# Kernel optimization log

Measured on AMD Instinct MI355X. Metric: run time of the kernel, lower is better.

The kernel has to match this reference:

```python
import jax, jax.numpy as jnp
import numpy as np

N_NODES = 50000
N_EDGES = 600000
N_GRAPHS = 512
IN_C, HID_C, OUT_C = 128, 128, 64


def setup_inputs() -> dict:
    key = jax.random.key(0)
    ks = jax.random.split(key, 16)
    inp = {
        "x": jax.random.normal(ks[0], (N_NODES, IN_C), dtype=jnp.float32),
        "edge_index": jax.random.randint(ks[1], (2, N_EDGES), 0, N_NODES, dtype=jnp.int64),
        "batch": jnp.sort(jax.random.randint(ks[2], (N_NODES,), 0, N_GRAPHS, dtype=jnp.int64)),
    }
    # GINConv MLPs: Linear(din,dout) -> ReLU -> Linear(dout,dout)
    dims = [(IN_C, HID_C), (HID_C, HID_C), (HID_C, OUT_C)]
    ki = 3
    for l, (din, dout) in enumerate(dims):
        inp[f"w1_{l}"] = jax.random.normal(ks[ki], (din, dout), jnp.float32) / np.sqrt(din).astype(np.float32)
        inp[f"b1_{l}"] = jnp.zeros((dout,), jnp.float32)
        inp[f"w2_{l}"] = jax.random.normal(ks[ki + 1], (dout, dout), jnp.float32) / np.sqrt(dout).astype(np.float32)
        inp[f"b2_{l}"] = jnp.zeros((dout,), jnp.float32)
        ki += 2
    return inp


def _gin_conv(x, src, dst, w1, b1, w2, b2):
    # sum-aggregate neighbor features: agg[i] = sum_{(j->i) in E} x[j]
    agg = jax.ops.segment_sum(x[src], dst, num_segments=N_NODES)
    h = x + agg  # eps = 0 -> (1+eps)*x + agg
    h = jnp.maximum(h @ w1 + b1, 0.0)
    return h @ w2 + b2


def reference(x, edge_index, batch,
              w1_0, b1_0, w2_0, b2_0,
              w1_1, b1_1, w2_1, b2_1,
              w1_2, b1_2, w2_2, b2_2):
    src, dst = edge_index[0], edge_index[1]
    params = [(w1_0, b1_0, w2_0, b2_0),
              (w1_1, b1_1, w2_1, b2_1),
              (w1_2, b1_2, w2_2, b2_2)]
    # first num_layers-1 convs with outer ReLU
    for l in range(2):
        x = jnp.maximum(_gin_conv(x, src, dst, *params[l]), 0.0)
    x = _gin_conv(x, src, dst, *params[2])
    # global_add_pool over graph ids -> [G, out_channels]
    return jax.ops.segment_sum(x, batch, num_segments=N_GRAPHS)
```

## Files before the change

kernel.cpp:

```cpp
#include <hip/hip_runtime.h>

#define N_NODES 50000
#define N_EDGES 600000
#define N_GRAPHS 512
#define CAP 48
#define NRT 3125

typedef unsigned int u32;
typedef unsigned short u16;
typedef __attribute__((ext_vector_type(8))) short bf16x8;
typedef __attribute__((ext_vector_type(4))) float f32x4;

__device__ __forceinline__ float bflo(u32 v) { return __uint_as_float(v << 16); }
__device__ __forceinline__ float bfhi(u32 v) { return __uint_as_float(v & 0xffff0000u); }
__device__ __forceinline__ u16 f2bf(float f) {
    u32 x = __float_as_uint(f);
    return (u16)((x + 0x7fffu + ((x >> 16) & 1u)) >> 16);
}
__device__ __forceinline__ void addrow(float* a, uint4 v) {
    a[0] += bflo(v.x); a[1] += bfhi(v.x);
    a[2] += bflo(v.y); a[3] += bfhi(v.y);
    a[4] += bflo(v.z); a[5] += bfhi(v.z);
    a[6] += bflo(v.w); a[7] += bfhi(v.w);
}
__device__ __forceinline__ void addrow2(float* a, uint2 v) {
    a[0] += bflo(v.x); a[1] += bfhi(v.x);
    a[2] += bflo(v.y); a[3] += bfhi(v.y);
}

__device__ __forceinline__ int idx_at(const int* __restrict__ a, int i, int wide) {
    return wide ? a[2 * i] : a[i];
}

__global__ void init_kernel(const int* __restrict__ ei, int* __restrict__ cnt,
                            int* __restrict__ flag, float* __restrict__ out,
                            int out_n) {
    int i = blockIdx.x * 256 + threadIdx.x;
    if (i < N_NODES) cnt[i] = 0;
    if (i < out_n) out[i] = 0.f;
    if (blockIdx.x == 0 && threadIdx.x < 64) {
        int v = ei[2 * threadIdx.x + 1];
        unsigned long long nz = __ballot(v != 0);
        if (threadIdx.x == 0) *flag = (nz == 0ull) ? 1 : 0;
    }
}

struct CvtDesc { const float* w; u16* wt; int K, N, bx, bstart; };
struct CvtAll { CvtDesc d[6]; };
struct PrepArgs {
    const int* ei; const int* flag;
    int* cnt; int* slots;
    const float* x; u16* xb;
    CvtAll ca;
};
#define SCAT_B 2344
#define CVTX_B 6250
#define PREP_B (SCAT_B + CVTX_B + 76)

__global__ void prep_kernel(PrepArgs p) {
    int b = blockIdx.x;
    if (b < SCAT_B) {
        int e = b * 256 + threadIdx.x;
        if (e >= N_EDGES) return;
        int w = *p.flag;
        const int* src = p.ei;
        const int* dst = p.ei + (w ? 2 * N_EDGES : N_EDGES);
        int d = idx_at(dst, e, w);
        int pos = atomicAdd(&p.cnt[d], 1);
        if (pos < CAP) p.slots[(size_t)d * CAP + pos] = idx_at(src, e, w);
        return;
    }
    if (b < SCAT_B + CVTX_B) {
        size_t i = (size_t)(b - SCAT_B) * 256 + threadIdx.x;
        float4 v = *(const float4*)&p.x[i * 4];
        u32 o0 = (u32)f2bf(v.x) | ((u32)f2bf(v.y) << 16);
        u32 o1 = (u32)f2bf(v.z) | ((u32)f2bf(v.w) << 16);
        uint2 o; o.x = o0; o.y = o1;
        *(uint2*)&p.xb[i * 4] = o;
        return;
    }
    __shared__ float tile[32][33];
    int rel0 = b - (SCAT_B + CVTX_B);
    int di = 0;
#pragma unroll
    for (int i = 1; i < 6; ++i) if (rel0 >= p.ca.d[i].bstart) di = i;
    CvtDesc d = p.ca.d[di];
    int rel = rel0 - d.bstart;
    int bk = (rel % d.bx) * 32, bn = (rel / d.bx) * 32;
    int tx = threadIdx.x & 31, ty = threadIdx.x >> 5;
#pragma unroll
    for (int yy = 0; yy < 32; yy += 8)
        tile[ty + yy][tx] = d.w[(size_t)(bk + ty + yy) * d.N + bn + tx];
    __syncthreads();
#pragma unroll
    for (int yy = 0; yy < 32; yy += 8)
        d.wt[(size_t)(bn + ty + yy) * d.K + bk + tx] = f2bf(tile[tx][ty + yy]);
}

__global__ void agg128_kernel(const u16* __restrict__ xb, const int* __restrict__ cnt,
                              const int* __restrict__ slots, u16* __restrict__ h2) {
    int node = blockIdx.x * 16 + (threadIdx.x >> 4);
    int l = threadIdx.x & 15;
    if (node >= N_NODES) return;
    uint4 sv = *(const uint4*)(xb + ((size_t)node << 7) + l * 8);
    float acc[8] = { bflo(sv.x), bfhi(sv.x), bflo(sv.y), bfhi(sv.y),
                     bflo(sv.z), bfhi(sv.z), bflo(sv.w), bfhi(sv.w) };
    int deg = cnt[node]; if (deg > CAP) deg = CAP;
    const int* sp = slots + (size_t)node * CAP;
    int j = 0;
    for (; j + 4 <= deg; j += 4) {
        int s0 = sp[j], s1 = sp[j + 1], s2 = sp[j + 2], s3 = sp[j + 3];
        uint4 v0 = *(const uint4*)(xb + ((size_t)s0 << 7) + l * 8);
        uint4 v1 = *(const uint4*)(xb + ((size_t)s1 << 7) + l * 8);
        uint4 v2 = *(const uint4*)(xb + ((size_t)s2 << 7) + l * 8);
        uint4 v3 = *(const uint4*)(xb + ((size_t)s3 << 7) + l * 8);
        addrow(acc, v0); addrow(acc, v1);
        addrow(acc, v2); addrow(acc, v3);
    }
    for (; j < deg; ++j) {
        int s0 = sp[j];
        uint4 v0 = *(const uint4*)(xb + ((size_t)s0 << 7) + l * 8);
        addrow(acc, v0);
    }
    uint4 o;
    o.x = (u32)f2bf(acc[0]) | ((u32)f2bf(acc[1]) << 16);
    o.y = (u32)f2bf(acc[2]) | ((u32)f2bf(acc[3]) << 16);
    o.z = (u32)f2bf(acc[4]) | ((u32)f2bf(acc[5]) << 16);
    o.w = (u32)f2bf(acc[6]) | ((u32)f2bf(acc[7]) << 16);
    *(uint4*)(h2 + (size_t)(node >> 4) * 2048 + l * 128 + (node & 15) * 8) = o;
}

__global__ void agg64_kernel(const u16* __restrict__ z, const int* __restrict__ cnt,
                             const int* __restrict__ slots,
                             const float* __restrict__ b1, u16* __restrict__ tout) {
    int node = blockIdx.x * 16 + (threadIdx.x >> 4);
    int l = threadIdx.x & 15;
    if (node >= N_NODES) return;
    uint2 sv = *(const uint2*)(z + ((size_t)node << 6) + l * 4);
    float acc[4] = { bflo(sv.x), bfhi(sv.x), bflo(sv.y), bfhi(sv.y) };
    int deg = cnt[node]; if (deg > CAP) deg = CAP;
    const int* sp = slots + (size_t)node * CAP;
    int j = 0;
    for (; j + 4 <= deg; j += 4) {
        int s0 = sp[j], s1 = sp[j + 1], s2 = sp[j + 2], s3 = sp[j + 3];
        uint2 v0 = *(const uint2*)(z + ((size_t)s0 << 6) + l * 4);
        uint2 v1 = *(const uint2*)(z + ((size_t)s1 << 6) + l * 4);
        uint2 v2 = *(const uint2*)(z + ((size_t)s2 << 6) + l * 4);
        uint2 v3 = *(const uint2*)(z + ((size_t)s3 << 6) + l * 4);
        addrow2(acc, v0); addrow2(acc, v1);
        addrow2(acc, v2); addrow2(acc, v3);
    }
    for (; j < deg; ++j) {
        int s0 = sp[j];
        uint2 v0 = *(const uint2*)(z + ((size_t)s0 << 6) + l * 4);
        addrow2(acc, v0);
    }
    float t0 = fmaxf(acc[0] + b1[l * 4 + 0], 0.f);
    float t1 = fmaxf(acc[1] + b1[l * 4 + 1], 0.f);
    float t2 = fmaxf(acc[2] + b1[l * 4 + 2], 0.f);
    float t3 = fmaxf(acc[3] + b1[l * 4 + 3], 0.f);
    uint2 o;
    o.x = (u32)f2bf(t0) | ((u32)f2bf(t1) << 16);
    o.y = (u32)f2bf(t2) | ((u32)f2bf(t3) << 16);
    *(uint2*)(tout + ((size_t)node << 6) + l * 4) = o;
}

template <int CHAIN>
__global__ __launch_bounds__(256) void mlp_kernel(
    const u16* __restrict__ h2,
    const u16* __restrict__ w1t, const float* __restrict__ b1,
    const u16* __restrict__ w2t, const float* __restrict__ b2,
    const u16* __restrict__ w3t, u16* __restrict__ zout,
    u16* __restrict__ yout)
{
    __shared__ __attribute__((aligned(16))) u16 ts[4 * 2048];
    __shared__ __attribute__((aligned(16))) u16 ys[4 * 2048];
    const int wave = threadIdx.x >> 6, lane = threadIdx.x & 63;
    const int rtile = blockIdx.x * 4 + wave;
    if (rtile >= NRT) return;
    const int m = lane & 15, q = lane >> 4, ko = q * 8;
    u16* tsw = ts + wave * 2048;
    u16* ysw = ys + wave * 2048;
    const u16* hp = h2 + (size_t)rtile * 2048;

    bf16x8 a1[4];
#pragma unroll
    for (int s = 0; s < 4; ++s)
        a1[s] = *(const bf16x8*)&hp[s * 512 + q * 128 + m * 8];

    {
        f32x4 acc[8];
#pragma unroll
        for (int nt = 0; nt < 8; ++nt) acc[nt] = (f32x4){0.f, 0.f, 0.f, 0.f};
#pragma unroll
        for (int nt = 0; nt < 8; ++nt) {
            int n = nt * 16 + m;
#pragma unroll
            for (int s = 0; s < 4; ++s) {
                bf16x8 bf = *(const bf16x8*)&w1t[(size_t)n * 128 + s * 32 + ko];
                acc[nt] = __builtin_amdgcn_mfma_f32_16x16x32_bf16(a1[s], bf, acc[nt], 0, 0, 0);
            }
        }
#pragma unroll
        for (int nt = 0; nt < 8; ++nt) {
            int n = nt * 16 + m;
            float bias = b1[n];
#pragma unroll
            for (int j2 = 0; j2 < 4; ++j2) {
                int dr = q * 4 + j2;
                float v = fmaxf(acc[nt][j2] + bias, 0.f);
                tsw[dr * 128 + (n ^ ((dr & 7) << 3))] = f2bf(v);
            }
        }
    }

    {
        const int sw = (m & 7) << 3;
        bf16x8 a2[4];
#pragma unroll
        for (int s = 0; s < 4; ++s)
            a2[s] = *(const bf16x8*)&tsw[m * 128 + ((s * 32 + ko) ^ sw)];
        f32x4 acc[8];
#pragma unroll
        for (int nt = 0; nt < 8; ++nt) acc[nt] = (f32x4){0.f, 0.f, 0.f, 0.f};
#pragma unroll
        for (int nt = 0; nt < 8; ++nt) {
            int n = nt * 16 + m;
#pragma unroll
            for (int s = 0; s < 4; ++s) {
                bf16x8 bf = *(const bf16x8*)&w2t[(size_t)n * 128 + s * 32 + ko];
                acc[nt] = __builtin_amdgcn_mfma_f32_16x16x32_bf16(a2[s], bf, acc[nt], 0, 0, 0);
            }
        }
#pragma unroll
        for (int nt = 0; nt < 8; ++nt) {
            int n = nt * 16 + m;
            float bias = b2[n];
#pragma unroll
            for (int j2 = 0; j2 < 4; ++j2) {
                int dr = q * 4 + j2;
                float v = fmaxf(acc[nt][j2] + bias, 0.f);
                ysw[dr * 128 + (n ^ ((dr & 7) << 3))] = f2bf(v);
            }
        }
    }

    if (CHAIN) {
        const int sw = (m & 7) << 3;
        bf16x8 a3[4];
#pragma unroll
        for (int s = 0; s < 4; ++s)
            a3[s] = *(const bf16x8*)&ysw[m * 128 + ((s * 32 + ko) ^ sw)];
        f32x4 acc3[4];
#pragma unroll
        for (int nt = 0; nt < 4; ++nt) acc3[nt] = (f32x4){0.f, 0.f, 0.f, 0.f};
#pragma unroll
        for (int nt = 0; nt < 4; ++nt) {
            int n3 = nt * 16 + m;
#pragma unroll
            for (int s = 0; s < 4; ++s) {
                bf16x8 bf = *(const bf16x8*)&w3t[(size_t)n3 * 128 + s * 32 + ko];
                acc3[nt] = __builtin_amdgcn_mfma_f32_16x16x32_bf16(a3[s], bf, acc3[nt], 0, 0, 0);
            }
        }
#pragma unroll
        for (int nt = 0; nt < 4; ++nt) {
            int n3 = nt * 16 + m;
#pragma unroll
            for (int j2 = 0; j2 < 4; ++j2) {
                int row = q * 4 + j2;
                zout[(size_t)(rtile * 16 + row) * 64 + n3] = f2bf(acc3[nt][j2]);
            }
        }
    } else {
        int r = lane >> 2;
        int c0 = (lane & 3) * 32;
        const int sw = (r & 7) << 3;
#pragma unroll
        for (int j = 0; j < 4; ++j) {
            int ce = c0 + j * 8;
            uint4 v = *(const uint4*)&ysw[r * 128 + (ce ^ sw)];
            *(uint4*)&yout[(size_t)(rtile * 16 + r) * 128 + ce] = v;
        }
    }
}

__global__ __launch_bounds__(1024) void pool_kernel(
    const u16* __restrict__ t, const u16* __restrict__ w2t,
    const float* __restrict__ b2,
    const int* __restrict__ batch, const int* __restrict__ flagp,
    float* __restrict__ out)
{
    constexpr int YB_ST = 66;
    __shared__ __attribute__((aligned(16))) char smemA[64 * YB_ST * 4];
    __shared__ int gids[64];
    u16* hs = (u16*)smemA;
    float* yb = (float*)smemA;

    const int tid = threadIdx.x;
    const int wave = tid >> 6, lane = tid & 63;
    const int base = blockIdx.x * 64;
    const int wflag = *flagp;

    if (tid < 64) {
        int node = base + tid;
        gids[tid] = (node < N_NODES) ? idx_at(batch, node, wflag) : -1;
    }
    {
        int row = tid >> 4, c0 = (tid & 15) * 4;
        uint2 v = *(const uint2*)&t[((size_t)(base + row)) * 64 + c0];
        *(uint2*)&hs[row * 64 + (c0 ^ ((row & 7) << 3))] = v;
    }
    __syncthreads();

    const int m = lane & 15;
    const int ko = (lane >> 4) * 8;
    const int rb = (wave & 3) * 16;
    const int cb = (wave >> 2) * 16;

    {
        const int rr = rb + m;
        const int sw = (rr & 7) << 3;
        bf16x8 a2[2];
#pragma unroll
        for (int s = 0; s < 2; ++s)
            a2[s] = *(const bf16x8*)&hs[rr * 64 + ((s * 32 + ko) ^ sw)];
        f32x4 acc = (f32x4){0.f, 0.f, 0.f, 0.f};
        int n = cb + m;
#pragma unroll
        for (int s = 0; s < 2; ++s) {
            bf16x8 bf = *(const bf16x8*)&w2t[(size_t)n * 64 + s * 32 + ko];
            acc = __builtin_amdgcn_mfma_f32_16x16x32_bf16(a2[s], bf, acc, 0, 0, 0);
        }
        float bias = b2[n];
        __syncthreads();
#pragma unroll
        for (int j2 = 0; j2 < 4; ++j2) {
            int dr = rb + (lane >> 4) * 4 + j2;
            yb[dr * YB_ST + n] = acc[j2] + bias;
        }
    }
    __syncthreads();

    {
        int gl = gids[lane];
        int gp = (lane > 0) ? gids[lane - 1] : gl;
        unsigned long long mask = __ballot(lane > 0 && gl != gp) | 1ull;
        int nruns = (int)__popcll(mask);
        int c = tid >> 4, s = tid & 15;
        unsigned long long mm = mask;
        for (int r = 0; r < nruns; ++r) {
            int start = (int)__builtin_ctzll(mm);
            mm &= mm - 1;
            int end = mm ? (int)__builtin_ctzll(mm) : 64;
            int gid = gids[start];
            if (gid >= 0) {
                float sum = 0.f;
                for (int n2 = start + s; n2 < end; n2 += 16)
                    sum += yb[n2 * YB_ST + c];
                sum += __shfl_xor(sum, 1);
                sum += __shfl_xor(sum, 2);
                sum += __shfl_xor(sum, 4);
                sum += __shfl_xor(sum, 8);
                if (s == 0)
                    atomicAdd(&out[(size_t)gid * 64 + c], sum);
            }
        }
    }
}

extern "C" void kernel_launch(void* const* d_in, const int* in_sizes, int n_in,
                              void* d_out, int out_size, void* d_ws, size_t ws_size,
                              hipStream_t stream) {
    const float* x     = (const float*)d_in[0];
    const int*   ei    = (const int*)d_in[1];
    const int*   batch = (const int*)d_in[2];
    const float* w1[3] = {(const float*)d_in[3], (const float*)d_in[7],  (const float*)d_in[11]};
    const float* b1[3] = {(const float*)d_in[4], (const float*)d_in[8],  (const float*)d_in[12]};
    const float* w2[3] = {(const float*)d_in[5], (const float*)d_in[9],  (const float*)d_in[13]};
    const float* b2[3] = {(const float*)d_in[6], (const float*)d_in[10], (const float*)d_in[14]};
    float* out = (float*)d_out;

    char* ws = (char*)d_ws;
    int*   cnt     = (int*)(ws + 0);
    int*   flag    = (int*)(ws + 200704);
    int*   slots   = (int*)(ws + 201728);
    u16*   xb      = (u16*)(ws + 9801728);
    u16*   hbuf    = (u16*)(ws + 22601728);
    u16*   yA      = (u16*)(ws + 35401728);
    u16*   wts     = (u16*)(ws + 48201728);
    u16*   zbuf    = xb;
    u16*   tbuf    = yA;
    u16* w1t0 = wts +      0;
    u16* w2t0 = wts +  16384;
    u16* w1t1 = wts +  32768;
    u16* w2t1 = wts +  49152;
    u16* w1t2 = wts +  65536;
    u16* w2t2 = wts +  73728;

    init_kernel<<<196, 256, 0, stream>>>(ei, cnt, flag, out, out_size);

    PrepArgs pa;
    pa.ei = ei; pa.flag = flag; pa.cnt = cnt; pa.slots = slots;
    pa.x = x; pa.xb = xb;
    pa.ca.d[0] = {w1[0], w1t0, 128, 128, 4,  0};
    pa.ca.d[1] = {w2[0], w2t0, 128, 128, 4, 16};
    pa.ca.d[2] = {w1[1], w1t1, 128, 128, 4, 32};
    pa.ca.d[3] = {w2[1], w2t1, 128, 128, 4, 48};
    pa.ca.d[4] = {w1[2], w1t2, 128,  64, 4, 64};
    pa.ca.d[5] = {w2[2], w2t2,  64,  64, 2, 72};
    prep_kernel<<<PREP_B, 256, 0, stream>>>(pa);

    const int NAGG = (N_NODES + 15) / 16;
    const int NTIL = (N_NODES + 63) / 64;

    agg128_kernel<<<NAGG, 256, 0, stream>>>(xb, cnt, slots, hbuf);
    mlp_kernel<0><<<NTIL, 256, 0, stream>>>(hbuf, w1t0, b1[0], w2t0, b2[0],
                                            (const u16*)0, (u16*)0, yA);
    agg128_kernel<<<NAGG, 256, 0, stream>>>(yA, cnt, slots, hbuf);
    mlp_kernel<1><<<NTIL, 256, 0, stream>>>(hbuf, w1t1, b1[1], w2t1, b2[1],
                                            w1t2, zbuf, (u16*)0);
    agg64_kernel<<<NAGG, 256, 0, stream>>>(zbuf, cnt, slots, b1[2], tbuf);
    pool_kernel<<<NTIL, 1024, 0, stream>>>(tbuf, w2t2, b2[2], batch, flag, out);
}
```

Measured before the change: 194.9 us.

## Use 16-bit neighbor slots and process two row tiles per wave in MLP

Neighbor index slots are stored as u16 instead of int, halving the bytes the aggregation kernels read and the scatter kernel writes. Node ids reach 49999, which fits in 16 bits. The MLP kernel now has each wave handle two 16-row tiles, so every weight fragment loaded from global memory feeds two MFMAs. It also reuses one LDS buffer in place of the separate t and y buffers. The cost is higher register pressure from doubled accumulators, and half as many blocks in the MLP launch.

```diff
diff --git a/kernel.cpp b/kernel.cpp
--- a/kernel.cpp
+++ b/kernel.cpp
@@ -49,7 +49,7 @@
 struct CvtAll { CvtDesc d[6]; };
 struct PrepArgs {
     const int* ei; const int* flag;
-    int* cnt; int* slots;
+    int* cnt; u16* slots;
     const float* x; u16* xb;
     CvtAll ca;
 };
@@ -67,7 +67,7 @@
         const int* dst = p.ei + (w ? 2 * N_EDGES : N_EDGES);
         int d = idx_at(dst, e, w);
         int pos = atomicAdd(&p.cnt[d], 1);
-        if (pos < CAP) p.slots[(size_t)d * CAP + pos] = idx_at(src, e, w);
+        if (pos < CAP) p.slots[(size_t)d * CAP + pos] = (u16)idx_at(src, e, w);
         return;
     }
     if (b < SCAT_B + CVTX_B) {
@@ -98,7 +98,7 @@
 }
 
 __global__ void agg128_kernel(const u16* __restrict__ xb, const int* __restrict__ cnt,
-                              const int* __restrict__ slots, u16* __restrict__ h2) {
+                              const u16* __restrict__ slots, u16* __restrict__ h2) {
     int node = blockIdx.x * 16 + (threadIdx.x >> 4);
     int l = threadIdx.x & 15;
     if (node >= N_NODES) return;
@@ -106,7 +106,7 @@
     float acc[8] = { bflo(sv.x), bfhi(sv.x), bflo(sv.y), bfhi(sv.y),
                      bflo(sv.z), bfhi(sv.z), bflo(sv.w), bfhi(sv.w) };
     int deg = cnt[node]; if (deg > CAP) deg = CAP;
-    const int* sp = slots + (size_t)node * CAP;
+    const u16* sp = slots + (size_t)node * CAP;
     int j = 0;
     for (; j + 4 <= deg; j += 4) {
         int s0 = sp[j], s1 = sp[j + 1], s2 = sp[j + 2], s3 = sp[j + 3];
@@ -131,7 +131,7 @@
 }
 
 __global__ void agg64_kernel(const u16* __restrict__ z, const int* __restrict__ cnt,
-                             const int* __restrict__ slots,
+                             const u16* __restrict__ slots,
                              const float* __restrict__ b1, u16* __restrict__ tout) {
     int node = blockIdx.x * 16 + (threadIdx.x >> 4);
     int l = threadIdx.x & 15;
@@ -139,7 +139,7 @@
     uint2 sv = *(const uint2*)(z + ((size_t)node << 6) + l * 4);
     float acc[4] = { bflo(sv.x), bfhi(sv.x), bflo(sv.y), bfhi(sv.y) };
     int deg = cnt[node]; if (deg > CAP) deg = CAP;
-    const int* sp = slots + (size_t)node * CAP;
+    const u16* sp = slots + (size_t)node * CAP;
     int j = 0;
     for (; j + 4 <= deg; j += 4) {
         int s0 = sp[j], s1 = sp[j + 1], s2 = sp[j + 2], s3 = sp[j + 3];
@@ -173,32 +173,44 @@
     const u16* __restrict__ w3t, u16* __restrict__ zout,
     u16* __restrict__ yout)
 {
-    __shared__ __attribute__((aligned(16))) u16 ts[4 * 2048];
-    __shared__ __attribute__((aligned(16))) u16 ys[4 * 2048];
+    __shared__ __attribute__((aligned(16))) u16 ls[4 * 4096];
     const int wave = threadIdx.x >> 6, lane = threadIdx.x & 63;
-    const int rtile = blockIdx.x * 4 + wave;
-    if (rtile >= NRT) return;
+    const int rtA = blockIdx.x * 8 + wave * 2;
+    const int rtB = rtA + 1;
+    if (rtA >= NRT) return;
+    const bool hasB = (rtB < NRT);
     const int m = lane & 15, q = lane >> 4, ko = q * 8;
-    u16* tsw = ts + wave * 2048;
-    u16* ysw = ys + wave * 2048;
-    const u16* hp = h2 + (size_t)rtile * 2048;
-
-    bf16x8 a1[4];
+    u16* tsA = ls + wave * 4096;
+    u16* tsB = tsA + 2048;
+    const u16* hpA = h2 + (size_t)rtA * 2048;
+    const u16* hpB = h2 + (size_t)rtB * 2048;
+
+    bf16x8 a1A[4], a1B[4];
 #pragma unroll
     for (int s = 0; s < 4; ++s)
-        a1[s] = *(const bf16x8*)&hp[s * 512 + q * 128 + m * 8];
+        a1A[s] = *(const bf16x8*)&hpA[s * 512 + q * 128 + m * 8];
+    if (hasB) {
+#pragma unroll
+        for (int s = 0; s < 4; ++s)
+            a1B[s] = *(const bf16x8*)&hpB[s * 512 + q * 128 + m * 8];
+    }
 
     {
-        f32x4 acc[8];
-#pragma unroll
-        for (int nt = 0; nt < 8; ++nt) acc[nt] = (f32x4){0.f, 0.f, 0.f, 0.f};
+        f32x4 accA[8], accB[8];
+#pragma unroll
+        for (int nt = 0; nt < 8; ++nt) {
+            accA[nt] = (f32x4){0.f, 0.f, 0.f, 0.f};
+            accB[nt] = (f32x4){0.f, 0.f, 0.f, 0.f};
+        }
 #pragma unroll
         for (int nt = 0; nt < 8; ++nt) {
             int n = nt * 16 + m;
 #pragma unroll
             for (int s = 0; s < 4; ++s) {
                 bf16x8 bf = *(const bf16x8*)&w1t[(size_t)n * 128 + s * 32 + ko];
-                acc[nt] = __builtin_amdgcn_mfma_f32_16x16x32_bf16(a1[s], bf, acc[nt], 0, 0, 0);
+                accA[nt] = __builtin_amdgcn_mfma_f32_16x16x32_bf16(a1A[s], bf, accA[nt], 0, 0, 0);
+                if (hasB)
+                    accB[nt] = __builtin_amdgcn_mfma_f32_16x16x32_bf16(a1B[s], bf, accB[nt], 0, 0, 0);
             }
         }
 #pragma unroll
@@ -208,28 +220,40 @@
 #pragma unroll
             for (int j2 = 0; j2 < 4; ++j2) {
                 int dr = q * 4 + j2;
-                float v = fmaxf(acc[nt][j2] + bias, 0.f);
-                tsw[dr * 128 + (n ^ ((dr & 7) << 3))] = f2bf(v);
+                int sw = (dr & 7) << 3;
+                tsA[dr * 128 + (n ^ sw)] = f2bf(fmaxf(accA[nt][j2] + bias, 0.f));
+                if (hasB)
+                    tsB[dr * 128 + (n ^ sw)] = f2bf(fmaxf(accB[nt][j2] + bias, 0.f));
             }
         }
     }
 
     {
-        const int sw = (m & 7) << 3;
-        bf16x8 a2[4];
+        const int swm = (m & 7) << 3;
+        bf16x8 a2A[4], a2B[4];
 #pragma unroll
         for (int s = 0; s < 4; ++s)
-            a2[s] = *(const bf16x8*)&tsw[m * 128 + ((s * 32 + ko) ^ sw)];
-        f32x4 acc[8];
-#pragma unroll
-        for (int nt = 0; nt < 8; ++nt) acc[nt] = (f32x4){0.f, 0.f, 0.f, 0.f};
+            a2A[s] = *(const bf16x8*)&tsA[m * 128 + ((s * 32 + ko) ^ swm)];
+        if (hasB) {
+#pragma unroll
+            for (int s = 0; s < 4; ++s)
+                a2B[s] = *(const bf16x8*)&tsB[m * 128 + ((s * 32 + ko) ^ swm)];
+        }
+        f32x4 accA[8], accB[8];
+#pragma unroll
+        for (int nt = 0; nt < 8; ++nt) {
+            accA[nt] = (f32x4){0.f, 0.f, 0.f, 0.f};
+            accB[nt] = (f32x4){0.f, 0.f, 0.f, 0.f};
+        }
 #pragma unroll
         for (int nt = 0; nt < 8; ++nt) {
             int n = nt * 16 + m;
 #pragma unroll
             for (int s = 0; s < 4; ++s) {
                 bf16x8 bf = *(const bf16x8*)&w2t[(size_t)n * 128 + s * 32 + ko];
-                acc[nt] = __builtin_amdgcn_mfma_f32_16x16x32_bf16(a2[s], bf, acc[nt], 0, 0, 0);
+                accA[nt] = __builtin_amdgcn_mfma_f32_16x16x32_bf16(a2A[s], bf, accA[nt], 0, 0, 0);
+                if (hasB)
+                    accB[nt] = __builtin_amdgcn_mfma_f32_16x16x32_bf16(a2B[s], bf, accB[nt], 0, 0, 0);
             }
         }
 #pragma unroll
@@ -239,28 +263,40 @@
 #pragma unroll
             for (int j2 = 0; j2 < 4; ++j2) {
                 int dr = q * 4 + j2;
-                float v = fmaxf(acc[nt][j2] + bias, 0.f);
-                ysw[dr * 128 + (n ^ ((dr & 7) << 3))] = f2bf(v);
+                int sw = (dr & 7) << 3;
+                tsA[dr * 128 + (n ^ sw)] = f2bf(fmaxf(accA[nt][j2] + bias, 0.f));
+                if (hasB)
+                    tsB[dr * 128 + (n ^ sw)] = f2bf(fmaxf(accB[nt][j2] + bias, 0.f));
             }
         }
     }
 
     if (CHAIN) {
-        const int sw = (m & 7) << 3;
-        bf16x8 a3[4];
+        const int swm = (m & 7) << 3;
+        bf16x8 a3A[4], a3B[4];
 #pragma unroll
         for (int s = 0; s < 4; ++s)
-            a3[s] = *(const bf16x8*)&ysw[m * 128 + ((s * 32 + ko) ^ sw)];
-        f32x4 acc3[4];
-#pragma unroll
-        for (int nt = 0; nt < 4; ++nt) acc3[nt] = (f32x4){0.f, 0.f, 0.f, 0.f};
+            a3A[s] = *(const bf16x8*)&tsA[m * 128 + ((s * 32 + ko) ^ swm)];
+        if (hasB) {
+#pragma unroll
+            for (int s = 0; s < 4; ++s)
+                a3B[s] = *(const bf16x8*)&tsB[m * 128 + ((s * 32 + ko) ^ swm)];
+        }
+        f32x4 accA[4], accB[4];
+#pragma unroll
+        for (int nt = 0; nt < 4; ++nt) {
+            accA[nt] = (f32x4){0.f, 0.f, 0.f, 0.f};
+            accB[nt] = (f32x4){0.f, 0.f, 0.f, 0.f};
+        }
 #pragma unroll
         for (int nt = 0; nt < 4; ++nt) {
             int n3 = nt * 16 + m;
 #pragma unroll
             for (int s = 0; s < 4; ++s) {
                 bf16x8 bf = *(const bf16x8*)&w3t[(size_t)n3 * 128 + s * 32 + ko];
-                acc3[nt] = __builtin_amdgcn_mfma_f32_16x16x32_bf16(a3[s], bf, acc3[nt], 0, 0, 0);
+                accA[nt] = __builtin_amdgcn_mfma_f32_16x16x32_bf16(a3A[s], bf, accA[nt], 0, 0, 0);
+                if (hasB)
+                    accB[nt] = __builtin_amdgcn_mfma_f32_16x16x32_bf16(a3B[s], bf, accB[nt], 0, 0, 0);
             }
         }
 #pragma unroll
@@ -269,7 +305,9 @@
 #pragma unroll
             for (int j2 = 0; j2 < 4; ++j2) {
                 int row = q * 4 + j2;
-                zout[(size_t)(rtile * 16 + row) * 64 + n3] = f2bf(acc3[nt][j2]);
+                zout[(size_t)(rtA * 16 + row) * 64 + n3] = f2bf(accA[nt][j2]);
+                if (hasB)
+                    zout[(size_t)(rtB * 16 + row) * 64 + n3] = f2bf(accB[nt][j2]);
             }
         }
     } else {
@@ -279,8 +317,16 @@
 #pragma unroll
         for (int j = 0; j < 4; ++j) {
             int ce = c0 + j * 8;
-            uint4 v = *(const uint4*)&ysw[r * 128 + (ce ^ sw)];
-            *(uint4*)&yout[(size_t)(rtile * 16 + r) * 128 + ce] = v;
+            uint4 v = *(const uint4*)&tsA[r * 128 + (ce ^ sw)];
+            *(uint4*)&yout[(size_t)(rtA * 16 + r) * 128 + ce] = v;
+        }
+        if (hasB) {
+#pragma unroll
+            for (int j = 0; j < 4; ++j) {
+                int ce = c0 + j * 8;
+                uint4 v = *(const uint4*)&tsB[r * 128 + (ce ^ sw)];
+                *(uint4*)&yout[(size_t)(rtB * 16 + r) * 128 + ce] = v;
+            }
         }
     }
 }
@@ -384,7 +430,7 @@
     char* ws = (char*)d_ws;
     int*   cnt     = (int*)(ws + 0);
     int*   flag    = (int*)(ws + 200704);
-    int*   slots   = (int*)(ws + 201728);
+    u16*   slots   = (u16*)(ws + 201728);
     u16*   xb      = (u16*)(ws + 9801728);
     u16*   hbuf    = (u16*)(ws + 22601728);
     u16*   yA      = (u16*)(ws + 35401728);
@@ -413,12 +459,13 @@
 
     const int NAGG = (N_NODES + 15) / 16;
     const int NTIL = (N_NODES + 63) / 64;
+    const int NMLP = (NRT + 7) / 8;
 
     agg128_kernel<<<NAGG, 256, 0, stream>>>(xb, cnt, slots, hbuf);
-    mlp_kernel<0><<<NTIL, 256, 0, stream>>>(hbuf, w1t0, b1[0], w2t0, b2[0],
+    mlp_kernel<0><<<NMLP, 256, 0, stream>>>(hbuf, w1t0, b1[0], w2t0, b2[0],
                                             (const u16*)0, (u16*)0, yA);
     agg128_kernel<<<NAGG, 256, 0, stream>>>(yA, cnt, slots, hbuf);
-    mlp_kernel<1><<<NTIL, 256, 0, stream>>>(hbuf, w1t1, b1[1], w2t1, b2[1],
+    mlp_kernel<1><<<NMLP, 256, 0, stream>>>(hbuf, w1t1, b1[1], w2t1, b2[1],
                                             w1t2, zbuf, (u16*)0);
     agg64_kernel<<<NAGG, 256, 0, stream>>>(zbuf, cnt, slots, b1[2], tbuf);
     pool_kernel<<<NTIL, 1024, 0, stream>>>(tbuf, w2t2, b2[2], batch, flag, out);
```

Result: faster. 174.4 us (-10.5%).
